# Kernel tuning notes

Measured on AMD Instinct MI355X. Metric: run time of the kernel, lower is better.

The kernel has to match this reference:

```python
import jax, jax.numpy as jnp
import numpy as np

N, E, G = 50000, 800000, 64
D_IN, D_H, D_OUT = 128, 256, 128
NEG_SLOPE = 0.01
BN_EPS = 1e-5


def setup_inputs() -> dict:
    key = jax.random.key(0)
    ks = jax.random.split(key, 20)
    x = jax.random.normal(ks[0], (N, D_IN), dtype=jnp.float32)
    edge_index = jax.random.randint(ks[1], (2, E), 0, N, dtype=jnp.int64)
    batch = jnp.sort(jax.random.randint(ks[2], (N,), 0, G, dtype=jnp.int64))
    dims = [(D_IN, D_H), (D_H, D_H), (D_H, D_H), (D_H, D_OUT)]
    inp = {"x": x, "edge_index": edge_index, "batch": batch}
    for i, (di, do) in enumerate(dims, start=1):
        s = 1.0 / np.sqrt(di)
        inp[f"W{i}"] = jax.random.normal(ks[3 + 4 * i], (di, do), dtype=jnp.float32) * s
        inp[f"b{i}"] = jnp.zeros((do,), dtype=jnp.float32)
        inp[f"g{i}"] = jnp.ones((do,), dtype=jnp.float32)
        inp[f"bt{i}"] = jnp.zeros((do,), dtype=jnp.float32)
    return inp


def _gcn_block(h, src, dst, norm, self_norm, W, b, g, bt):
    # GCNConv: h' = D^-1/2 (A+I) D^-1/2 (h W) + b  (degrees include self-loops)
    h = h @ W                                                    # [N, do]
    agg = jax.ops.segment_sum(h[src] * norm[:, None], dst, num_segments=N)
    h = agg + h * self_norm[:, None] + b
    # LeakyReLU then BatchNorm (batch statistics, as in training-mode BN)
    h = jnp.where(h > 0, h, NEG_SLOPE * h)
    mu = h.mean(axis=0)
    var = ((h - mu) ** 2).mean(axis=0)
    return (h - mu) * jax.lax.rsqrt(var + BN_EPS) * g + bt


def reference(x, edge_index, batch, W1, b1, g1, bt1, W2, b2, g2, bt2,
              W3, b3, g3, bt3, W4, b4, g4, bt4):
    src, dst = edge_index[0], edge_index[1]
    deg = jax.ops.segment_sum(jnp.ones((E,), x.dtype), dst, num_segments=N) + 1.0
    dinv = jax.lax.rsqrt(deg)                 # [N]
    norm = dinv[src] * dinv[dst]              # [E] edge normalization
    self_norm = 1.0 / deg                     # [N] self-loop normalization
    h = _gcn_block(x, src, dst, norm, self_norm, W1, b1, g1, bt1)
    h = _gcn_block(h, src, dst, norm, self_norm, W2, b2, g2, bt2)
    h = _gcn_block(h, src, dst, norm, self_norm, W3, b3, g3, bt3)
    h = _gcn_block(h, src, dst, norm, self_norm, W4, b4, g4, bt4)
    # global mean pool over graphs
    counts = jax.ops.segment_sum(jnp.ones((N,), h.dtype), batch, num_segments=G)
    sums = jax.ops.segment_sum(h, batch, num_segments=G)
    return sums / jnp.maximum(counts, 1.0)[:, None]   # [G, D_OUT]
```

## Files before the change

kernel.cpp:

```cpp
#include <hip/hip_runtime.h>
#include <hip/hip_bf16.h>

#define NEG_SLOPE 0.01f
#define BN_EPS 1e-5f
#define POOL_S 16

typedef __attribute__((ext_vector_type(8))) short short8;
typedef __attribute__((ext_vector_type(4))) float f32x4;

__device__ __forceinline__ float bf2f(unsigned short b) {
    unsigned int u = ((unsigned int)b) << 16;
    float f; __builtin_memcpy(&f, &u, 4); return f;
}
__device__ __forceinline__ unsigned short f2bf(float f) {
    unsigned int u; __builtin_memcpy(&u, &f, 4);
    u = (u + 0x7FFFu + ((u >> 16) & 1u)) >> 16;
    return (unsigned short)u;
}

__device__ __forceinline__ void gload_lds16(const void* g, void* l) {
    __builtin_amdgcn_global_load_lds(
        (const __attribute__((address_space(1))) void*)g,
        (__attribute__((address_space(3))) void*)l, 16, 0, 0);
}

__global__ void k_cvt(const float* __restrict__ x, unsigned short* __restrict__ xb, int total8) {
    int i = blockIdx.x * blockDim.x + threadIdx.x;
    if (i < total8) {
        float4 a = ((const float4*)x)[i * 2];
        float4 b = ((const float4*)x)[i * 2 + 1];
        short8 o;
        o[0] = (short)f2bf(a.x); o[1] = (short)f2bf(a.y);
        o[2] = (short)f2bf(a.z); o[3] = (short)f2bf(a.w);
        o[4] = (short)f2bf(b.x); o[5] = (short)f2bf(b.y);
        o[6] = (short)f2bf(b.z); o[7] = (short)f2bf(b.w);
        ((short8*)xb)[i] = o;
    }
}

__global__ void k_count(const int* __restrict__ ei, int* __restrict__ cnt, int E) {
    int e0 = (blockIdx.x * blockDim.x + threadIdx.x) * 4;
    if (e0 + 3 < E) {
        int4 d = *(const int4*)(ei + E + e0);
        atomicAdd(&cnt[d.x], 1);
        atomicAdd(&cnt[d.y], 1);
        atomicAdd(&cnt[d.z], 1);
        atomicAdd(&cnt[d.w], 1);
    } else {
        for (int e = e0; e < E; ++e) atomicAdd(&cnt[ei[E + e]], 1);
    }
}

__global__ __launch_bounds__(256) void k_scan1(const int* __restrict__ cnt,
                                               int* __restrict__ bsum,
                                               float* __restrict__ dinv, int n) {
    int b = blockIdx.x;
    int t = threadIdx.x;
    int base = b * 1024 + t * 4;
    int s = 0;
    #pragma unroll
    for (int i = 0; i < 4; ++i) {
        int v = (base + i < n) ? cnt[base + i] : 0;
        if (base + i < n) dinv[base + i] = rsqrtf((float)(v + 1));
        s += v;
    }
    #pragma unroll
    for (int off = 1; off < 64; off <<= 1) s += __shfl_xor(s, off, 64);
    __shared__ int ws[4];
    if ((t & 63) == 0) ws[t >> 6] = s;
    __syncthreads();
    if (t == 0) bsum[b] = ws[0] + ws[1] + ws[2] + ws[3];
}

__global__ void k_scan2(const int* __restrict__ bsum, int* __restrict__ boff,
                        int* __restrict__ row_ptr, int nb, int n) {
    int lane = threadIdx.x;
    int v = (lane < nb) ? bsum[lane] : 0;
    int x = v;
    #pragma unroll
    for (int off = 1; off < 64; off <<= 1) {
        int t = __shfl_up(x, off, 64);
        if (lane >= off) x += t;
    }
    if (lane < nb) boff[lane] = x - v;
    if (lane == 63) row_ptr[n] = x;
}

__global__ __launch_bounds__(256) void k_scan3(const int* __restrict__ cnt,
                                               const int* __restrict__ boff,
                                               int* __restrict__ row_ptr, int n) {
    int b = blockIdx.x;
    int t = threadIdx.x;
    int lane = t & 63, w = t >> 6;
    int base = b * 1024 + t * 4;
    int v[4];
    #pragma unroll
    for (int i = 0; i < 4; ++i) v[i] = (base + i < n) ? cnt[base + i] : 0;
    int tsum = v[0] + v[1] + v[2] + v[3];
    int x = tsum;
    #pragma unroll
    for (int off = 1; off < 64; off <<= 1) {
        int tt = __shfl_up(x, off, 64);
        if (lane >= off) x += tt;
    }
    __shared__ int ws[4];
    if (lane == 63) ws[w] = x;
    __syncthreads();
    int woff = 0;
    for (int k = 0; k < 4; ++k) if (k < w) woff += ws[k];
    int excl = boff[b] + woff + x - tsum;
    #pragma unroll
    for (int i = 0; i < 4; ++i) {
        if (base + i < n) row_ptr[base + i] = excl;
        excl += v[i];
    }
}

__global__ void k_fill(const int* __restrict__ ei, const int* __restrict__ row_ptr,
                       int* __restrict__ cnt, int* __restrict__ eidx, int E) {
    int e0 = (blockIdx.x * blockDim.x + threadIdx.x) * 4;
    if (e0 + 3 < E) {
        int4 s = *(const int4*)(ei + e0);
        int4 d = *(const int4*)(ei + E + e0);
        int p0 = atomicSub(&cnt[d.x], 1) - 1;
        int p1 = atomicSub(&cnt[d.y], 1) - 1;
        int p2 = atomicSub(&cnt[d.z], 1) - 1;
        int p3 = atomicSub(&cnt[d.w], 1) - 1;
        eidx[row_ptr[d.x] + p0] = s.x;
        eidx[row_ptr[d.y] + p1] = s.y;
        eidx[row_ptr[d.z] + p2] = s.z;
        eidx[row_ptr[d.w] + p3] = s.w;
    } else {
        for (int e = e0; e < E; ++e) {
            int src = ei[e];
            int dst = ei[E + e];
            int pos = atomicSub(&cnt[dst], 1) - 1;
            eidx[row_ptr[dst] + pos] = src;
        }
    }
}

__global__ void k_init_affine(float* __restrict__ s, float* __restrict__ sh,
                              float* __restrict__ sums) {
    int c = threadIdx.x;
    s[c] = 1.0f;
    sh[c] = 0.0f;
    sums[c] = 0.f;
    sums[256 + c] = 0.f;
}

__global__ void k_prepW(const float* __restrict__ W, const float* __restrict__ scale,
                        unsigned short* __restrict__ Wt, int K, int DO) {
    int idx = blockIdx.x * blockDim.x + threadIdx.x;
    if (idx < K * DO) {
        int k = idx / DO, n = idx % DO;
        float v = W[idx];
        if (scale) v *= scale[k];
        Wt[(size_t)n * K + k] = f2bf(v);
    }
}

__global__ __launch_bounds__(256) void k_prepd(const float* __restrict__ W,
                                               const float* __restrict__ sh,
                                               float* __restrict__ d, int K, int DO) {
    int c = blockIdx.x;
    int t = threadIdx.x;
    float a = (t < K) ? sh[t] * W[(size_t)t * DO + c] : 0.f;
    #pragma unroll
    for (int off = 1; off < 64; off <<= 1) a += __shfl_xor(a, off, 64);
    __shared__ float ws[4];
    if ((t & 63) == 0) ws[t >> 6] = a;
    __syncthreads();
    if (t == 0) d[c] = ws[0] + ws[1] + ws[2] + ws[3];
}

template<int COLS, bool EPI>
__global__ __launch_bounds__(256) void k_aggw(const unsigned short* __restrict__ h,
    const float* __restrict__ s, const float* __restrict__ sh,
    const float* __restrict__ dv, const float* __restrict__ bias,
    const int* __restrict__ row_ptr, const int* __restrict__ eidx,
    const float* __restrict__ dinv, unsigned short* __restrict__ t, int N) {
    constexpr int LPR = COLS / 8;
    constexpr int GR  = 64 / LPR;
    constexpr int SH  = (COLS == 256) ? 8 : 7;
    int n = blockIdx.x * 4 + (threadIdx.x >> 6);
    if (n >= N) return;
    int l = threadIdx.x & 63;
    int ct = l & (LPR - 1);
    int gp = l / LPR;
    const unsigned short* up = h + ct * 8;
    int b = row_ptr[n], e = row_ptr[n + 1];
    int cnt = e - b;
    int per = (cnt + GR - 1) / GR;
    int jb = b + gp * per;
    int je = min(jb + per, e);
    float dn = dinv[n];
    float acc[8] = {};
    float ssum = 0.f;
    if (gp == 0) {
        short8 hv = *(const short8*)(up + ((size_t)n << SH));
        #pragma unroll
        for (int i = 0; i < 8; ++i) acc[i] += dn * bf2f((unsigned short)hv[i]);
    }
    int j = jb;
    for (; j + 4 <= je; j += 4) {
        int s0 = eidx[j], s1 = eidx[j + 1], s2 = eidx[j + 2], s3 = eidx[j + 3];
        float d0 = dinv[s0], d1 = dinv[s1], d2 = dinv[s2], d3 = dinv[s3];
        short8 r0 = *(const short8*)(up + ((size_t)s0 << SH));
        short8 r1 = *(const short8*)(up + ((size_t)s1 << SH));
        short8 r2 = *(const short8*)(up + ((size_t)s2 << SH));
        short8 r3 = *(const short8*)(up + ((size_t)s3 << SH));
        ssum += (d0 + d1) + (d2 + d3);
        #pragma unroll
        for (int i = 0; i < 8; ++i) {
            float a01 = d0 * bf2f((unsigned short)r0[i]) + d1 * bf2f((unsigned short)r1[i]);
            float a23 = d2 * bf2f((unsigned short)r2[i]) + d3 * bf2f((unsigned short)r3[i]);
            acc[i] += a01 + a23;
        }
    }
    for (; j < je; ++j) {
        int s0 = eidx[j];
        float d0 = dinv[s0];
        ssum += d0;
        short8 r0 = *(const short8*)(up + ((size_t)s0 << SH));
        #pragma unroll
        for (int i = 0; i < 8; ++i) acc[i] += d0 * bf2f((unsigned short)r0[i]);
    }
    #pragma unroll
    for (int mask = LPR; mask < 64; mask <<= 1) {
        #pragma unroll
        for (int i = 0; i < 8; ++i) acc[i] += __shfl_xor(acc[i], mask, 64);
        ssum += __shfl_xor(ssum, mask, 64);
    }
    if (gp == 0) {
        float ws = dn * ssum + dn * dn;
        short8 ov;
        #pragma unroll
        for (int i = 0; i < 8; ++i) {
            int col = ct * 8 + i;
            float o;
            if constexpr (EPI) {
                o = dn * acc[i] + ws * dv[col] + bias[col];
                o = o > 0.f ? o : NEG_SLOPE * o;
            } else {
                o = s[col] * (dn * acc[i]) + sh[col] * ws;
            }
            ov[i] = (short)f2bf(o);
        }
        *(short8*)(t + ((size_t)n << SH) + ct * 8) = ov;
    }
}

template<int K, int DO, bool FUSE>
__global__ __launch_bounds__(256) void k_mfma2(
    const unsigned short* __restrict__ A, const unsigned short* __restrict__ Wt,
    const float* __restrict__ bias, unsigned short* __restrict__ H,
    float* __restrict__ sums, int M) {
    __shared__ unsigned short Asm[128 * 64];
    __shared__ unsigned short Bsm[128 * 64];
    __shared__ float ls[2][128];
    int tid = threadIdx.x;
    int l = tid & 63, w = tid >> 6;
    int wr = w & 1, wc = w >> 1;
    int rl = l & 15, kh = l >> 4;
    int Rb = blockIdx.x * 128;
    int Cb = blockIdx.y * 128;
    int srow = tid >> 3;
    int sd   = tid & 7;
    f32x4 acc[4][4] = {};
    for (int k0 = 0; k0 < K; k0 += 64) {
        #pragma unroll
        for (int i = 0; i < 4; ++i) {
            int row = i * 32 + srow;
            int ss = sd ^ (row & 7);
            int rg = Rb + row; if (rg >= M) rg = M - 1;
            gload_lds16(A + (size_t)rg * K + k0 + ss * 8,
                        (char*)Asm + i * 4096 + w * 1024);
            gload_lds16(Wt + (size_t)(Cb + row) * K + k0 + ss * 8,
                        (char*)Bsm + i * 4096 + w * 1024);
        }
        __syncthreads();
        #pragma unroll
        for (int kk = 0; kk < 2; ++kk) {
            short8 af[4], bf[4];
            #pragma unroll
            for (int mf = 0; mf < 4; ++mf) {
                int r = wr * 64 + mf * 16 + rl;
                int slot = (kk * 4 + kh) ^ (r & 7);
                af[mf] = *(const short8*)((const char*)Asm + r * 128 + slot * 16);
            }
            #pragma unroll
            for (int nf = 0; nf < 4; ++nf) {
                int c = wc * 64 + nf * 16 + rl;
                int slot = (kk * 4 + kh) ^ (c & 7);
                bf[nf] = *(const short8*)((const char*)Bsm + c * 128 + slot * 16);
            }
            #pragma unroll
            for (int mf = 0; mf < 4; ++mf)
                #pragma unroll
                for (int nf = 0; nf < 4; ++nf)
                    acc[mf][nf] = __builtin_amdgcn_mfma_f32_16x16x32_bf16(
                        af[mf], bf[nf], acc[mf][nf], 0, 0, 0);
        }
        __syncthreads();
    }
    if constexpr (FUSE) {
        for (int c = tid; c < 128; c += 256) { ls[0][c] = 0.f; ls[1][c] = 0.f; }
        __syncthreads();
    }
    #pragma unroll
    for (int nf = 0; nf < 4; ++nf) {
        int cl = wc * 64 + nf * 16 + rl;
        int col = Cb + cl;
        float bcol = FUSE ? bias[col] : 0.f;
        float p1 = 0.f, p2 = 0.f;
        #pragma unroll
        for (int mf = 0; mf < 4; ++mf) {
            #pragma unroll
            for (int r = 0; r < 4; ++r) {
                int row = Rb + wr * 64 + mf * 16 + kh * 4 + r;
                if (row < M) {
                    if constexpr (FUSE) {
                        float z = acc[mf][nf][r] + bcol;
                        z = z > 0.f ? z : NEG_SLOPE * z;
                        H[(size_t)row * DO + col] = f2bf(z);
                        p1 += z; p2 += z * z;
                    } else {
                        H[(size_t)row * DO + col] = f2bf(acc[mf][nf][r]);
                    }
                }
            }
        }
        if constexpr (FUSE) {
            atomicAdd(&ls[0][cl], p1);
            atomicAdd(&ls[1][cl], p2);
        }
    }
    if constexpr (FUSE) {
        __syncthreads();
        for (int c = tid; c < 128; c += 256) {
            atomicAdd(&sums[Cb + c], ls[0][c]);
            atomicAdd(&sums[256 + Cb + c], ls[1][c]);
        }
    }
}

__global__ void k_stats_bf(const unsigned short* __restrict__ h, float* __restrict__ sums, int M) {
    int c = threadIdx.x;
    float s1 = 0.f, s2 = 0.f;
    for (int r = blockIdx.x; r < M; r += gridDim.x) {
        float v = bf2f(h[(size_t)r * 128 + c]);
        s1 += v; s2 += v * v;
    }
    atomicAdd(&sums[c], s1);
    atomicAdd(&sums[256 + c], s2);
}

__global__ void k_finalize(float* __restrict__ sums, const float* __restrict__ g,
                           const float* __restrict__ bt, float* __restrict__ s_out,
                           float* __restrict__ sh_out, float Nf) {
    int c = threadIdx.x;
    float mu = sums[c] / Nf;
    float var = sums[256 + c] / Nf - mu * mu;
    float rs = rsqrtf(var + BN_EPS);
    float sc = g[c] * rs;
    s_out[c] = sc;
    sh_out[c] = bt[c] - mu * sc;
    sums[c] = 0.f;
    sums[256 + c] = 0.f;
}

__global__ void k_pool1(const unsigned short* __restrict__ h, const int* __restrict__ batch,
                        float* __restrict__ part, int N) {
    int g = blockIdx.x;
    int sidx = blockIdx.y;
    int c = threadIdx.x;
    int lo = 0, hi = N;
    while (lo < hi) { int m = (lo + hi) >> 1; if (batch[m] < g) lo = m + 1; else hi = m; }
    int start = lo; hi = N;
    while (lo < hi) { int m = (lo + hi) >> 1; if (batch[m] < g + 1) lo = m + 1; else hi = m; }
    int end = lo;
    float acc = 0.f;
    for (int r = start + sidx; r < end; r += POOL_S)
        acc += bf2f(h[(size_t)r * 128 + c]);
    part[((size_t)g * POOL_S + sidx) * 128 + c] = acc;
}

__global__ void k_pool2(const float* __restrict__ part, const int* __restrict__ batch,
                        const float* __restrict__ s, const float* __restrict__ sh,
                        float* __restrict__ out, int N) {
    int g = blockIdx.x;
    int c = threadIdx.x;
    int lo = 0, hi = N;
    while (lo < hi) { int m = (lo + hi) >> 1; if (batch[m] < g) lo = m + 1; else hi = m; }
    int start = lo; hi = N;
    while (lo < hi) { int m = (lo + hi) >> 1; if (batch[m] < g + 1) lo = m + 1; else hi = m; }
    int cnt = lo - start;
    float acc = 0.f;
    #pragma unroll
    for (int i = 0; i < POOL_S; ++i) acc += part[((size_t)g * POOL_S + i) * 128 + c];
    out[(size_t)g * 128 + c] = (cnt > 0) ? (s[c] * acc / (float)cnt + sh[c]) : 0.f;
}


static inline size_t align256(size_t x) { return (x + 255) & ~(size_t)255; }

extern "C" void kernel_launch(void* const* d_in, const int* in_sizes, int n_in,
                              void* d_out, int out_size, void* d_ws, size_t ws_size,
                              hipStream_t stream) {
    const float* x   = (const float*)d_in[0];
    const int* ei    = (const int*)d_in[1];
    const int* batch = (const int*)d_in[2];
    const float* Wp[4]  = {(const float*)d_in[3], (const float*)d_in[7],
                           (const float*)d_in[11], (const float*)d_in[15]};
    const float* bp[4]  = {(const float*)d_in[4], (const float*)d_in[8],
                           (const float*)d_in[12], (const float*)d_in[16]};
    const float* gp[4]  = {(const float*)d_in[5], (const float*)d_in[9],
                           (const float*)d_in[13], (const float*)d_in[17]};
    const float* btp[4] = {(const float*)d_in[6], (const float*)d_in[10],
                           (const float*)d_in[14], (const float*)d_in[18]};

    const int N = in_sizes[0] / 128;
    const int E = in_sizes[1] / 2;
    const int G = out_size / 128;

    char* p = (char*)d_ws;
    int* deg_cnt = (int*)p;            p += align256((size_t)N * 4);
    int* row_ptr = (int*)p;            p += align256((size_t)(N + 1) * 4);
    float* dinv = (float*)p;           p += align256((size_t)N * 4);
    int* bsum = (int*)p;               p += align256(64 * 4);
    int* boff = (int*)p;               p += align256(64 * 4);
    int* eidx = (int*)p;               p += align256((size_t)E * 4);
    float* sums = (float*)p;           p += align256(512 * 4);
    float* s_arr = (float*)p;          p += align256(5 * 256 * 4);
    float* sh_arr = (float*)p;         p += align256(5 * 256 * 4);
    float* dvec = (float*)p;           p += align256(256 * 4);
    unsigned short* Wt = (unsigned short*)p; p += align256(256 * 256 * 2);
    float* part = (float*)p;           p += align256((size_t)G * POOL_S * 128 * 4);
    unsigned short* xb = (unsigned short*)p;   p += align256((size_t)N * 128 * 2);
    unsigned short* bufA = (unsigned short*)p; p += align256((size_t)N * 256 * 2);
    unsigned short* bufB = (unsigned short*)p; p += align256((size_t)N * 256 * 2);

    k_cvt<<<(N * 128 / 8 + 255) / 256, 256, 0, stream>>>(x, xb, N * 128 / 8);

    hipMemsetAsync(deg_cnt, 0, (size_t)N * 4, stream);
    k_count<<<(E / 4 + 255) / 256, 256, 0, stream>>>(ei, deg_cnt, E);
    const int nb = (N + 1023) / 1024;
    k_scan1<<<nb, 256, 0, stream>>>(deg_cnt, bsum, dinv, N);
    k_scan2<<<1, 64, 0, stream>>>(bsum, boff, row_ptr, nb, N);
    k_scan3<<<nb, 256, 0, stream>>>(deg_cnt, boff, row_ptr, N);
    k_fill<<<(E / 4 + 255) / 256, 256, 0, stream>>>(ei, row_ptr, deg_cnt, eidx, E);
    k_init_affine<<<1, 256, 0, stream>>>(s_arr, sh_arr, sums);

    const int ablocks = (N + 3) / 4;
    const int gx = (N + 127) / 128;

    k_aggw<128, false><<<ablocks, 256, 0, stream>>>(xb, s_arr, sh_arr, nullptr, nullptr,
        row_ptr, eidx, dinv, bufA, N);
    k_prepW<<<(128 * 256 + 255) / 256, 256, 0, stream>>>(Wp[0], nullptr, Wt, 128, 256);
    k_mfma2<128, 256, true><<<dim3(gx, 2), 256, 0, stream>>>(bufA, Wt, bp[0], bufB, sums, N);
    k_finalize<<<1, 256, 0, stream>>>(sums, gp[0], btp[0], s_arr + 256, sh_arr + 256, (float)N);

    for (int L = 1; L <= 2; ++L) {
        k_aggw<256, false><<<ablocks, 256, 0, stream>>>(bufB, s_arr + L * 256, sh_arr + L * 256,
            nullptr, nullptr, row_ptr, eidx, dinv, bufA, N);
        k_prepW<<<(256 * 256 + 255) / 256, 256, 0, stream>>>(Wp[L], nullptr, Wt, 256, 256);
        k_mfma2<256, 256, true><<<dim3(gx, 2), 256, 0, stream>>>(bufA, Wt, bp[L], bufB, sums, N);
        k_finalize<<<1, 256, 0, stream>>>(sums, gp[L], btp[L],
                                          s_arr + (L + 1) * 256, sh_arr + (L + 1) * 256, (float)N);
    }

    k_prepW<<<(256 * 128 + 255) / 256, 256, 0, stream>>>(Wp[3], s_arr + 3 * 256, Wt, 256, 128);
    k_prepd<<<128, 256, 0, stream>>>(Wp[3], sh_arr + 3 * 256, dvec, 256, 128);
    k_mfma2<256, 128, false><<<dim3(gx, 1), 256, 0, stream>>>(bufB, Wt, nullptr, bufA, nullptr, N);
    k_aggw<128, true><<<ablocks, 256, 0, stream>>>(bufA, nullptr, nullptr, dvec, bp[3],
        row_ptr, eidx, dinv, bufB, N);
    k_stats_bf<<<256, 128, 0, stream>>>(bufB, sums, N);
    k_finalize<<<1, 128, 0, stream>>>(sums, gp[3], btp[3], s_arr + 4 * 256, sh_arr + 4 * 256, (float)N);

    dim3 pgrid(G, POOL_S);
    k_pool1<<<pgrid, 128, 0, stream>>>(bufB, batch, part, N);
    k_pool2<<<G, 128, 0, stream>>>(part, batch, s_arr + 4 * 256, sh_arr + 4 * 256,
                                   (float*)d_out, N);
}
```

Before: 517.2 us.

## Pre-scale features by dinv, pad CSR rows to multiples of four, fuse stats into pooling

Stores each node's features already multiplied by its dinv, so the aggregation loop drops the per-edge dinv gathers and multiplies. The per-node weighted neighbour sum of dinv is computed once in a new kernel. CSR rows are padded to multiples of four with a sentinel node whose zeroed feature row contributes nothing, which allows int4 index loads and removes the tail loop. The final BatchNorm statistics pass is folded into the pooling kernel. In exchange it adds padding, zeroing and sum kernels, slightly more memory, and the sentinel rows must stay zero in every buffer that is gathered from.

```diff
diff --git a/kernel.cpp b/kernel.cpp
--- a/kernel.cpp
+++ b/kernel.cpp
@@ -24,16 +24,18 @@
         (__attribute__((address_space(3))) void*)l, 16, 0, 0);
 }
 
-__global__ void k_cvt(const float* __restrict__ x, unsigned short* __restrict__ xb, int total8) {
+__global__ void k_cvt(const float* __restrict__ x, const float* __restrict__ dinv,
+                      unsigned short* __restrict__ xb, int total8) {
     int i = blockIdx.x * blockDim.x + threadIdx.x;
     if (i < total8) {
+        float dn = dinv[i >> 4];
         float4 a = ((const float4*)x)[i * 2];
         float4 b = ((const float4*)x)[i * 2 + 1];
         short8 o;
-        o[0] = (short)f2bf(a.x); o[1] = (short)f2bf(a.y);
-        o[2] = (short)f2bf(a.z); o[3] = (short)f2bf(a.w);
-        o[4] = (short)f2bf(b.x); o[5] = (short)f2bf(b.y);
-        o[6] = (short)f2bf(b.z); o[7] = (short)f2bf(b.w);
+        o[0] = (short)f2bf(dn * a.x); o[1] = (short)f2bf(dn * a.y);
+        o[2] = (short)f2bf(dn * a.z); o[3] = (short)f2bf(dn * a.w);
+        o[4] = (short)f2bf(dn * b.x); o[5] = (short)f2bf(dn * b.y);
+        o[6] = (short)f2bf(dn * b.z); o[7] = (short)f2bf(dn * b.w);
         ((short8*)xb)[i] = o;
     }
 }
@@ -56,13 +58,16 @@
                                                float* __restrict__ dinv, int n) {
     int b = blockIdx.x;
     int t = threadIdx.x;
+    if (b == 0 && t == 0) dinv[n] = 0.f;
     int base = b * 1024 + t * 4;
     int s = 0;
     #pragma unroll
     for (int i = 0; i < 4; ++i) {
-        int v = (base + i < n) ? cnt[base + i] : 0;
-        if (base + i < n) dinv[base + i] = rsqrtf((float)(v + 1));
-        s += v;
+        if (base + i < n) {
+            int v = cnt[base + i];
+            dinv[base + i] = rsqrtf((float)(v + 1));
+            s += (v + 3) & ~3;
+        }
     }
     #pragma unroll
     for (int off = 1; off < 64; off <<= 1) s += __shfl_xor(s, off, 64);
@@ -95,7 +100,8 @@
     int base = b * 1024 + t * 4;
     int v[4];
     #pragma unroll
-    for (int i = 0; i < 4; ++i) v[i] = (base + i < n) ? cnt[base + i] : 0;
+    for (int i = 0; i < 4; ++i)
+        v[i] = (base + i < n) ? ((cnt[base + i] + 3) & ~3) : 0;
     int tsum = v[0] + v[1] + v[2] + v[3];
     int x = tsum;
     #pragma unroll
@@ -113,6 +119,16 @@
     for (int i = 0; i < 4; ++i) {
         if (base + i < n) row_ptr[base + i] = excl;
         excl += v[i];
+    }
+}
+
+__global__ void k_pad(const int* __restrict__ cnt, const int* __restrict__ row_ptr,
+                      int* __restrict__ eidx, int N) {
+    int n = blockIdx.x * blockDim.x + threadIdx.x;
+    if (n < N) {
+        int s = row_ptr[n] + cnt[n];
+        int e = row_ptr[n + 1];
+        for (int j = s; j < e; ++j) eidx[j] = N;
     }
 }
 
@@ -140,6 +156,37 @@
     }
 }
 
+__global__ void k_zero(unsigned short* __restrict__ xb, unsigned short* __restrict__ bufA,
+                       unsigned short* __restrict__ bufB, int N) {
+    int t = threadIdx.x;
+    if (t < 128) xb[(size_t)N * 128 + t] = 0;
+    if (t < 128) bufA[(size_t)N * 128 + t] = 0;
+    bufB[(size_t)N * 256 + t] = 0;
+}
+
+__global__ void k_zeroA128(unsigned short* __restrict__ bufA, int N) {
+    int t = threadIdx.x;
+    bufA[(size_t)N * 128 + t] = 0;
+}
+
+__global__ __launch_bounds__(256) void k_ssum(const int* __restrict__ row_ptr,
+                                              const int* __restrict__ eidx,
+                                              const float* __restrict__ dinv,
+                                              float* __restrict__ S, int N) {
+    int n = blockIdx.x * 4 + (threadIdx.x >> 6);
+    if (n >= N) return;
+    int l = threadIdx.x & 63;
+    int b = row_ptr[n], e = row_ptr[n + 1];
+    float s = 0.f;
+    for (int j = b + l * 4; j < e; j += 256) {
+        int4 sv = *(const int4*)(eidx + j);
+        s += (dinv[sv.x] + dinv[sv.y]) + (dinv[sv.z] + dinv[sv.w]);
+    }
+    #pragma unroll
+    for (int off = 1; off < 64; off <<= 1) s += __shfl_xor(s, off, 64);
+    if (l == 0) S[n] = s;
+}
+
 __global__ void k_init_affine(float* __restrict__ s, float* __restrict__ sh,
                               float* __restrict__ sums) {
     int c = threadIdx.x;
@@ -179,7 +226,8 @@
     const float* __restrict__ s, const float* __restrict__ sh,
     const float* __restrict__ dv, const float* __restrict__ bias,
     const int* __restrict__ row_ptr, const int* __restrict__ eidx,
-    const float* __restrict__ dinv, unsigned short* __restrict__ t, int N) {
+    const float* __restrict__ dinv, const float* __restrict__ S,
+    unsigned short* __restrict__ t, int N) {
     constexpr int LPR = COLS / 8;
     constexpr int GR  = 64 / LPR;
     constexpr int SH  = (COLS == 256) ? 8 : 7;
@@ -190,50 +238,37 @@
     int gp = l / LPR;
     const unsigned short* up = h + ct * 8;
     int b = row_ptr[n], e = row_ptr[n + 1];
-    int cnt = e - b;
-    int per = (cnt + GR - 1) / GR;
+    int cnt4 = e - b;
+    int per = (((cnt4 + GR - 1) / GR) + 3) & ~3;
     int jb = b + gp * per;
     int je = min(jb + per, e);
-    float dn = dinv[n];
     float acc[8] = {};
-    float ssum = 0.f;
     if (gp == 0) {
         short8 hv = *(const short8*)(up + ((size_t)n << SH));
         #pragma unroll
-        for (int i = 0; i < 8; ++i) acc[i] += dn * bf2f((unsigned short)hv[i]);
-    }
-    int j = jb;
-    for (; j + 4 <= je; j += 4) {
-        int s0 = eidx[j], s1 = eidx[j + 1], s2 = eidx[j + 2], s3 = eidx[j + 3];
-        float d0 = dinv[s0], d1 = dinv[s1], d2 = dinv[s2], d3 = dinv[s3];
-        short8 r0 = *(const short8*)(up + ((size_t)s0 << SH));
-        short8 r1 = *(const short8*)(up + ((size_t)s1 << SH));
-        short8 r2 = *(const short8*)(up + ((size_t)s2 << SH));
-        short8 r3 = *(const short8*)(up + ((size_t)s3 << SH));
-        ssum += (d0 + d1) + (d2 + d3);
+        for (int i = 0; i < 8; ++i) acc[i] += bf2f((unsigned short)hv[i]);
+    }
+    for (int j = jb; j < je; j += 4) {
+        int4 sv = *(const int4*)(eidx + j);
+        short8 r0 = *(const short8*)(up + ((size_t)sv.x << SH));
+        short8 r1 = *(const short8*)(up + ((size_t)sv.y << SH));
+        short8 r2 = *(const short8*)(up + ((size_t)sv.z << SH));
+        short8 r3 = *(const short8*)(up + ((size_t)sv.w << SH));
         #pragma unroll
         for (int i = 0; i < 8; ++i) {
-            float a01 = d0 * bf2f((unsigned short)r0[i]) + d1 * bf2f((unsigned short)r1[i]);
-            float a23 = d2 * bf2f((unsigned short)r2[i]) + d3 * bf2f((unsigned short)r3[i]);
+            float a01 = bf2f((unsigned short)r0[i]) + bf2f((unsigned short)r1[i]);
+            float a23 = bf2f((unsigned short)r2[i]) + bf2f((unsigned short)r3[i]);
             acc[i] += a01 + a23;
         }
     }
-    for (; j < je; ++j) {
-        int s0 = eidx[j];
-        float d0 = dinv[s0];
-        ssum += d0;
-        short8 r0 = *(const short8*)(up + ((size_t)s0 << SH));
-        #pragma unroll
-        for (int i = 0; i < 8; ++i) acc[i] += d0 * bf2f((unsigned short)r0[i]);
-    }
     #pragma unroll
     for (int mask = LPR; mask < 64; mask <<= 1) {
         #pragma unroll
         for (int i = 0; i < 8; ++i) acc[i] += __shfl_xor(acc[i], mask, 64);
-        ssum += __shfl_xor(ssum, mask, 64);
     }
     if (gp == 0) {
-        float ws = dn * ssum + dn * dn;
+        float dn = dinv[n];
+        float ws = dn * S[n] + dn * dn;
         short8 ov;
         #pragma unroll
         for (int i = 0; i < 8; ++i) {
@@ -254,8 +289,8 @@
 template<int K, int DO, bool FUSE>
 __global__ __launch_bounds__(256) void k_mfma2(
     const unsigned short* __restrict__ A, const unsigned short* __restrict__ Wt,
-    const float* __restrict__ bias, unsigned short* __restrict__ H,
-    float* __restrict__ sums, int M) {
+    const float* __restrict__ bias, const float* __restrict__ dinv,
+    unsigned short* __restrict__ H, float* __restrict__ sums, int M) {
     __shared__ unsigned short Asm[128 * 64];
     __shared__ unsigned short Bsm[128 * 64];
     __shared__ float ls[2][128];
@@ -307,53 +342,50 @@
     if constexpr (FUSE) {
         for (int c = tid; c < 128; c += 256) { ls[0][c] = 0.f; ls[1][c] = 0.f; }
         __syncthreads();
-    }
-    #pragma unroll
-    for (int nf = 0; nf < 4; ++nf) {
-        int cl = wc * 64 + nf * 16 + rl;
-        int col = Cb + cl;
-        float bcol = FUSE ? bias[col] : 0.f;
-        float p1 = 0.f, p2 = 0.f;
+        float p1[4] = {}, p2[4] = {};
         #pragma unroll
         for (int mf = 0; mf < 4; ++mf) {
             #pragma unroll
             for (int r = 0; r < 4; ++r) {
                 int row = Rb + wr * 64 + mf * 16 + kh * 4 + r;
                 if (row < M) {
-                    if constexpr (FUSE) {
-                        float z = acc[mf][nf][r] + bcol;
+                    float dr = dinv[row];
+                    #pragma unroll
+                    for (int nf = 0; nf < 4; ++nf) {
+                        int col = Cb + wc * 64 + nf * 16 + rl;
+                        float z = acc[mf][nf][r] + bias[col];
                         z = z > 0.f ? z : NEG_SLOPE * z;
-                        H[(size_t)row * DO + col] = f2bf(z);
-                        p1 += z; p2 += z * z;
-                    } else {
-                        H[(size_t)row * DO + col] = f2bf(acc[mf][nf][r]);
+                        H[(size_t)row * DO + col] = f2bf(dr * z);
+                        p1[nf] += z; p2[nf] += z * z;
                     }
                 }
             }
         }
-        if constexpr (FUSE) {
-            atomicAdd(&ls[0][cl], p1);
-            atomicAdd(&ls[1][cl], p2);
-        }
-    }
-    if constexpr (FUSE) {
+        #pragma unroll
+        for (int nf = 0; nf < 4; ++nf) {
+            int cl = wc * 64 + nf * 16 + rl;
+            atomicAdd(&ls[0][cl], p1[nf]);
+            atomicAdd(&ls[1][cl], p2[nf]);
+        }
         __syncthreads();
         for (int c = tid; c < 128; c += 256) {
             atomicAdd(&sums[Cb + c], ls[0][c]);
             atomicAdd(&sums[256 + Cb + c], ls[1][c]);
         }
-    }
-}
-
-__global__ void k_stats_bf(const unsigned short* __restrict__ h, float* __restrict__ sums, int M) {
-    int c = threadIdx.x;
-    float s1 = 0.f, s2 = 0.f;
-    for (int r = blockIdx.x; r < M; r += gridDim.x) {
-        float v = bf2f(h[(size_t)r * 128 + c]);
-        s1 += v; s2 += v * v;
-    }
-    atomicAdd(&sums[c], s1);
-    atomicAdd(&sums[256 + c], s2);
+    } else {
+        #pragma unroll
+        for (int nf = 0; nf < 4; ++nf) {
+            int col = Cb + wc * 64 + nf * 16 + rl;
+            #pragma unroll
+            for (int mf = 0; mf < 4; ++mf) {
+                #pragma unroll
+                for (int r = 0; r < 4; ++r) {
+                    int row = Rb + wr * 64 + mf * 16 + kh * 4 + r;
+                    if (row < M) H[(size_t)row * DO + col] = f2bf(acc[mf][nf][r]);
+                }
+            }
+        }
+    }
 }
 
 __global__ void k_finalize(float* __restrict__ sums, const float* __restrict__ g,
@@ -371,7 +403,7 @@
 }
 
 __global__ void k_pool1(const unsigned short* __restrict__ h, const int* __restrict__ batch,
-                        float* __restrict__ part, int N) {
+                        float* __restrict__ part, float* __restrict__ sums, int N) {
     int g = blockIdx.x;
     int sidx = blockIdx.y;
     int c = threadIdx.x;
@@ -380,10 +412,14 @@
     int start = lo; hi = N;
     while (lo < hi) { int m = (lo + hi) >> 1; if (batch[m] < g + 1) lo = m + 1; else hi = m; }
     int end = lo;
-    float acc = 0.f;
-    for (int r = start + sidx; r < end; r += POOL_S)
-        acc += bf2f(h[(size_t)r * 128 + c]);
+    float acc = 0.f, sq = 0.f;
+    for (int r = start + sidx; r < end; r += POOL_S) {
+        float v = bf2f(h[(size_t)r * 128 + c]);
+        acc += v; sq += v * v;
+    }
     part[((size_t)g * POOL_S + sidx) * 128 + c] = acc;
+    atomicAdd(&sums[c], acc);
+    atomicAdd(&sums[256 + c], sq);
 }
 
 __global__ void k_pool2(const float* __restrict__ part, const int* __restrict__ batch,
@@ -427,21 +463,20 @@
     char* p = (char*)d_ws;
     int* deg_cnt = (int*)p;            p += align256((size_t)N * 4);
     int* row_ptr = (int*)p;            p += align256((size_t)(N + 1) * 4);
-    float* dinv = (float*)p;           p += align256((size_t)N * 4);
+    float* dinv = (float*)p;           p += align256((size_t)(N + 1) * 4);
+    float* Svec = (float*)p;           p += align256((size_t)N * 4);
     int* bsum = (int*)p;               p += align256(64 * 4);
     int* boff = (int*)p;               p += align256(64 * 4);
-    int* eidx = (int*)p;               p += align256((size_t)E * 4);
+    int* eidx = (int*)p;               p += align256((size_t)(E + 3 * (N + 1)) * 4);
     float* sums = (float*)p;           p += align256(512 * 4);
     float* s_arr = (float*)p;          p += align256(5 * 256 * 4);
     float* sh_arr = (float*)p;         p += align256(5 * 256 * 4);
     float* dvec = (float*)p;           p += align256(256 * 4);
     unsigned short* Wt = (unsigned short*)p; p += align256(256 * 256 * 2);
     float* part = (float*)p;           p += align256((size_t)G * POOL_S * 128 * 4);
-    unsigned short* xb = (unsigned short*)p;   p += align256((size_t)N * 128 * 2);
-    unsigned short* bufA = (unsigned short*)p; p += align256((size_t)N * 256 * 2);
-    unsigned short* bufB = (unsigned short*)p; p += align256((size_t)N * 256 * 2);
-
-    k_cvt<<<(N * 128 / 8 + 255) / 256, 256, 0, stream>>>(x, xb, N * 128 / 8);
+    unsigned short* xb = (unsigned short*)p;   p += align256((size_t)(N + 1) * 128 * 2);
+    unsigned short* bufA = (unsigned short*)p; p += align256((size_t)(N + 1) * 256 * 2);
+    unsigned short* bufB = (unsigned short*)p; p += align256((size_t)(N + 1) * 256 * 2);
 
     hipMemsetAsync(deg_cnt, 0, (size_t)N * 4, stream);
     k_count<<<(E / 4 + 255) / 256, 256, 0, stream>>>(ei, deg_cnt, E);
@@ -449,37 +484,41 @@
     k_scan1<<<nb, 256, 0, stream>>>(deg_cnt, bsum, dinv, N);
     k_scan2<<<1, 64, 0, stream>>>(bsum, boff, row_ptr, nb, N);
     k_scan3<<<nb, 256, 0, stream>>>(deg_cnt, boff, row_ptr, N);
+    k_pad<<<(N + 255) / 256, 256, 0, stream>>>(deg_cnt, row_ptr, eidx, N);
     k_fill<<<(E / 4 + 255) / 256, 256, 0, stream>>>(ei, row_ptr, deg_cnt, eidx, E);
+    k_zero<<<1, 256, 0, stream>>>(xb, bufA, bufB, N);
+    k_ssum<<<(N + 3) / 4, 256, 0, stream>>>(row_ptr, eidx, dinv, Svec, N);
+    k_cvt<<<(N * 128 / 8 + 255) / 256, 256, 0, stream>>>(x, dinv, xb, N * 128 / 8);
     k_init_affine<<<1, 256, 0, stream>>>(s_arr, sh_arr, sums);
 
     const int ablocks = (N + 3) / 4;
     const int gx = (N + 127) / 128;
 
     k_aggw<128, false><<<ablocks, 256, 0, stream>>>(xb, s_arr, sh_arr, nullptr, nullptr,
-        row_ptr, eidx, dinv, bufA, N);
+        row_ptr, eidx, dinv, Svec, bufA, N);
     k_prepW<<<(128 * 256 + 255) / 256, 256, 0, stream>>>(Wp[0], nullptr, Wt, 128, 256);
-    k_mfma2<128, 256, true><<<dim3(gx, 2), 256, 0, stream>>>(bufA, Wt, bp[0], bufB, sums, N);
+    k_mfma2<128, 256, true><<<dim3(gx, 2), 256, 0, stream>>>(bufA, Wt, bp[0], dinv, bufB, sums, N);
     k_finalize<<<1, 256, 0, stream>>>(sums, gp[0], btp[0], s_arr + 256, sh_arr + 256, (float)N);
 
     for (int L = 1; L <= 2; ++L) {
         k_aggw<256, false><<<ablocks, 256, 0, stream>>>(bufB, s_arr + L * 256, sh_arr + L * 256,
-            nullptr, nullptr, row_ptr, eidx, dinv, bufA, N);
+            nullptr, nullptr, row_ptr, eidx, dinv, Svec, bufA, N);
         k_prepW<<<(256 * 256 + 255) / 256, 256, 0, stream>>>(Wp[L], nullptr, Wt, 256, 256);
-        k_mfma2<256, 256, true><<<dim3(gx, 2), 256, 0, stream>>>(bufA, Wt, bp[L], bufB, sums, N);
+        k_mfma2<256, 256, true><<<dim3(gx, 2), 256, 0, stream>>>(bufA, Wt, bp[L], dinv, bufB, sums, N);
         k_finalize<<<1, 256, 0, stream>>>(sums, gp[L], btp[L],
                                           s_arr + (L + 1) * 256, sh_arr + (L + 1) * 256, (float)N);
     }
 
+    k_zeroA128<<<1, 128, 0, stream>>>(bufA, N);
+
     k_prepW<<<(256 * 128 + 255) / 256, 256, 0, stream>>>(Wp[3], s_arr + 3 * 256, Wt, 256, 128);
     k_prepd<<<128, 256, 0, stream>>>(Wp[3], sh_arr + 3 * 256, dvec, 256, 128);
-    k_mfma2<256, 128, false><<<dim3(gx, 1), 256, 0, stream>>>(bufB, Wt, nullptr, bufA, nullptr, N);
+    k_mfma2<256, 128, false><<<dim3(gx, 1), 256, 0, stream>>>(bufB, Wt, nullptr, dinv, bufA, nullptr, N);
     k_aggw<128, true><<<ablocks, 256, 0, stream>>>(bufA, nullptr, nullptr, dvec, bp[3],
-        row_ptr, eidx, dinv, bufB, N);
-    k_stats_bf<<<256, 128, 0, stream>>>(bufB, sums, N);
+        row_ptr, eidx, dinv, Svec, bufB, N);
+    dim3 pgrid(G, POOL_S);
+    k_pool1<<<pgrid, 128, 0, stream>>>(bufB, batch, part, sums, N);
     k_finalize<<<1, 128, 0, stream>>>(sums, gp[3], btp[3], s_arr + 4 * 256, sh_arr + 4 * 256, (float)N);
-
-    dim3 pgrid(G, POOL_S);
-    k_pool1<<<pgrid, 128, 0, stream>>>(bufB, batch, part, N);
     k_pool2<<<G, 128, 0, stream>>>(part, batch, s_arr + 4 * 256, sh_arr + 4 * 256,
                                    (float*)d_out, N);
 }
```

Measured after the change: 489.8 us. 1.06x faster.
